# Kernel optimization log

Hardware: AMD Instinct MI355X
Metric: run time of the kernel (lower is better)

The kernel has to match this reference:

```python
import jax, jax.numpy as jnp
import numpy as np

B = 1      # batch
D = 64     # octree grid side at this level
N = 65536  # active voxels
C = 32     # channels (nin == nout for resblock)
K = 3      # kernel size


def _offsets():
    r = jnp.arange(K) - K // 2
    oz, oy, ox = jnp.meshgrid(r, r, r, indexing='ij')
    return jnp.stack([oz.ravel(), oy.ravel(), ox.ravel()], axis=-1)  # [27,3] (kz,ky,kx order)


def octree_conv3d(values, indices, mask_values, kernel, bias, activation=None):
    # values: [N,Cin], indices: [N,4] (b,z,y,x), mask_values: [N,1]
    Cin = values.shape[-1]
    Cout = kernel.shape[-1]
    taps = kernel.reshape(K * K * K, Cin, Cout)            # kz,ky,kx order == kernel[kz,ky,kx]
    vals = jnp.einsum('nc,tcd->tnd', values, taps)         # [27,N,Cout]
    offs = _offsets()                                      # [27,3]
    coords = indices[:, 1:]                                # [N,3]
    # shift = [0, kz-1, ky-1, kx-1]; clamp to [0, D-1] (stride=inv_stride=1)
    sh = jnp.clip(coords[None, :, :] + offs[:, None, :], 0, D - 1)  # [27,N,3]
    lin = indices[:, 0][None, :] * (D * D * D) + sh[..., 0] * (D * D) + sh[..., 1] * D + sh[..., 2]
    grid = jnp.zeros((B * D * D * D, Cout), dtype=values.dtype)
    grid = grid.at[lin.reshape(-1)].add(vals.reshape(-1, Cout))     # scatter-add == coalesce sum
    out_lin = indices[:, 0] * (D * D * D) + coords[:, 0] * (D * D) + coords[:, 1] * D + coords[:, 2]
    gathered = grid[out_lin]                               # [N,Cout] values at mask positions
    out = (gathered + mask_values * bias[None, :]) * mask_values     # result + mask*bias; result*mask
    if activation is not None:
        out = activation(out)
    return out


def setup_inputs() -> dict:
    key = jax.random.key(0)
    k1, k2, k3, k4, k5, k6 = jax.random.split(key, 6)
    G = B * D * D * D
    perm = jax.random.permutation(k1, G)[:N]               # unique (coalesced) voxel indices
    b = perm // (D * D * D)
    rem = perm % (D * D * D)
    z = rem // (D * D)
    y = (rem // D) % D
    x = rem % D
    indices = jnp.stack([b, z, y, x], axis=-1).astype(jnp.int64)   # [N,4]
    values = jax.random.normal(k2, (N, C), dtype=jnp.float32)
    mask_values = jnp.ones((N, 1), dtype=jnp.float32)
    stdv = 1.0 / np.sqrt(K * K * K * C)
    kern1 = (jax.random.uniform(k3, (K, K, K, C, C)) - 0.5) * 2.0 * stdv
    bias1 = (jax.random.uniform(k4, (C,)) - 0.5) * 2.0 * stdv
    kern2 = (jax.random.uniform(k5, (K, K, K, C, C)) - 0.5) * 2.0 * stdv
    bias2 = (jax.random.uniform(k6, (C,)) - 0.5) * 2.0 * stdv
    return {'values': values, 'indices': indices, 'mask_values': mask_values,
            'kern1': kern1, 'bias1': bias1, 'kern2': kern2, 'bias2': bias2}


def reference(values, indices, mask_values, kern1, bias1, kern2, bias2):
    # OctreeResblock: conv(relu) -> conv -> residual add, all on the sparse index set
    h = octree_conv3d(values, indices, mask_values, kern1, bias1, activation=jax.nn.relu)
    h = octree_conv3d(h, indices, mask_values, kern2, bias2, activation=None)
    return values + h
```

## Files before the change

kernel.cpp:

```cpp
#include <hip/hip_runtime.h>
#include <hip/hip_cooperative_groups.h>

namespace cg = cooperative_groups;

#define NPTS 65536
#define CCH  32
#define DDIM 64
#define GVOX (DDIM*DDIM*DDIM)
#define MAXTILES 4128
#define NTHREADS 1024
#define NBLOCKS  256
#define TTOT (NTHREADS*NBLOCKS)

typedef _Float16 half8  __attribute__((ext_vector_type(8)));
typedef _Float16 half4v __attribute__((ext_vector_type(4)));
typedef float    floatx4 __attribute__((ext_vector_type(4)));

#define P0N (GVOX/4 + MAXTILES*16 + (NPTS*CCH)/4 + 27*CCH*CCH + CCH + 27 + 1)

struct SharedC {
  _Float16 lw[27*CCH*CCH];
  int tstart[28];
  int clsbase[27];
  int lcnt[27];
  int lbase[27];
};

template<int MODE>
__device__ void conv_phase_c(SharedC& sh,
    const _Float16* __restrict__ A, const int* __restrict__ map,
    const int* __restrict__ pcoord, const int* __restrict__ sorted,
    const _Float16* __restrict__ WT, const float* __restrict__ bias,
    const float* __restrict__ mask, const float* __restrict__ resid,
    _Float16* __restrict__ hout, float* __restrict__ fout)
{
  for (int i = threadIdx.x; i < (27*CCH*CCH)/8; i += NTHREADS)
    ((half8*)sh.lw)[i] = ((const half8*)WT)[i];
  __syncthreads();

  const int wv   = threadIdx.x >> 6;
  const int lane = threadIdx.x & 63;
  const int m = lane & 15, quad = lane >> 4;
  const int nt = sh.tstart[27];
  const float bi0 = bias[m], bi1 = bias[m+16];

  for (int tile = blockIdx.x*(NTHREADS/64) + wv; tile < nt;
       tile += NBLOCKS*(NTHREADS/64)) {
    int scls = 0;
    for (int cc = 1; cc < 27; ++cc) if (tile >= sh.tstart[cc]) scls = cc;
    scls = __builtin_amdgcn_readfirstlane(scls);
    const int cz = scls/9, cy = (scls/3)%3, cx = scls%3;

    const int pid = sorted[tile*16 + m];
    const int pc  = pcoord[pid];
    const int bb = pc>>18, z = (pc>>12)&63, y = (pc>>6)&63, x = pc&63;
    const int linb = bb << 18;
    const int az[3] = { max(z-1,0)<<12, z<<12, min(z+1,DDIM-1)<<12 };
    const int ay[3] = { max(y-1,0)<<6,  y<<6,  min(y+1,DDIM-1)<<6 };
    const int ax[3] = { max(x-1,0),     x,     min(x+1,DDIM-1) };

    floatx4 acc0 = {0.f,0.f,0.f,0.f};
    floatx4 acc1 = {0.f,0.f,0.f,0.f};

    int srcs[27];
#pragma unroll
    for (int j = 0; j < 27; ++j) {
      const int jz = j/9, jy = (j/3)%3, jx = j%3;
      const int s = map[linb | az[jz] | ay[jy] | ax[jx]];
      srcs[j] = (s < 0) ? (NPTS*CCH) : (s*CCH);
    }
#pragma unroll
    for (int j = 0; j < 27; ++j) {
      const int jz = j/9, jy = (j/3)%3, jx = j%3;
      const int tz = (cz==1) ? (2-jz) : ((jz==1) ? 1 : ((cz==0) ? 0 : 2));
      const int ty = (cy==1) ? (2-jy) : ((jy==1) ? 1 : ((cy==0) ? 0 : 2));
      const int tx = (cx==1) ? (2-jx) : ((jx==1) ? 1 : ((cx==0) ? 0 : 2));
      const int t  = tz*9 + ty*3 + tx;
      half8 a  = *(const half8*)(A + srcs[j] + quad*8);
      const _Float16* wr = sh.lw + t*(CCH*CCH);
      half8 b0 = *(const half8*)(wr + m*CCH + quad*8);
      half8 b1 = *(const half8*)(wr + (16+m)*CCH + quad*8);
      acc0 = __builtin_amdgcn_mfma_f32_16x16x32_f16(a, b0, acc0, 0, 0, 0);
      acc1 = __builtin_amdgcn_mfma_f32_16x16x32_f16(a, b1, acc1, 0, 0, 0);
    }

#pragma unroll
    for (int reg = 0; reg < 4; ++reg) {
      const int r  = quad*4 + reg;
      const int pr = sorted[tile*16 + r];
      if (pr >= NPTS) continue;
      const float mk = mask[pr];
      float v0 = (acc0[reg] + mk*bi0) * mk;
      float v1 = (acc1[reg] + mk*bi1) * mk;
      if (MODE == 0) {
        v0 = fmaxf(v0, 0.f); v1 = fmaxf(v1, 0.f);
        hout[pr*CCH + m]      = (_Float16)v0;
        hout[pr*CCH + m + 16] = (_Float16)v1;
      } else {
        fout[pr*CCH + m]      = resid[pr*CCH + m]      + v0;
        fout[pr*CCH + m + 16] = resid[pr*CCH + m + 16] + v1;
      }
    }
  }
}

__global__ __launch_bounds__(1024, 4) void mega2(
    const float* __restrict__ values, const int* __restrict__ idx,
    const float* __restrict__ maskv,
    const float* __restrict__ k1, const float* __restrict__ bias1,
    const float* __restrict__ k2, const float* __restrict__ bias2,
    int* __restrict__ map, int* __restrict__ pcoord,
    int* __restrict__ sorted, int* __restrict__ cnt, int* __restrict__ slot,
    _Float16* __restrict__ valsh, _Float16* __restrict__ hh,
    _Float16* __restrict__ wt1, _Float16* __restrict__ wt2,
    float* __restrict__ out)
{
  __shared__ SharedC sh;
  cg::grid_group grid = cg::this_grid();
  const int gtid = blockIdx.x*NTHREADS + threadIdx.x;

  for (int t0 = gtid; t0 < P0N; t0 += TTOT) {
    int tid = t0;
    if (tid < GVOX/4) { ((int4*)map)[tid] = make_int4(-1,-1,-1,-1); continue; }
    tid -= GVOX/4;
    if (tid < MAXTILES*16) { sorted[tid] = NPTS; continue; }
    tid -= MAXTILES*16;
    if (tid < (NPTS*CCH)/4) {
      float4 v = ((const float4*)values)[tid];
      half4v h = { (_Float16)v.x, (_Float16)v.y, (_Float16)v.z, (_Float16)v.w };
      ((half4v*)valsh)[tid] = h; continue;
    }
    tid -= (NPTS*CCH)/4;
    if (tid < 27*CCH*CCH) {
      int t = tid/(CCH*CCH), r = tid%(CCH*CCH);
      int cin = r/CCH, cout = r%CCH;
      int o = (t*CCH + cout)*CCH + cin;
      wt1[o] = (_Float16)k1[tid]; wt2[o] = (_Float16)k2[tid]; continue;
    }
    tid -= 27*CCH*CCH;
    if (tid < CCH) { valsh[NPTS*CCH+tid] = (_Float16)0.f; hh[NPTS*CCH+tid] = (_Float16)0.f; continue; }
    tid -= CCH;
    if (tid < 27) { cnt[tid] = 0; slot[tid] = 0; continue; }
    tid -= 27;
    if (tid == 0) pcoord[NPTS] = 0;
  }
  grid.sync();

  if (threadIdx.x < 27) sh.lcnt[threadIdx.x] = 0;
  __syncthreads();
  int myc = -1;
  if (gtid < NPTS) {
    const int4 v = ((const int4*)idx)[gtid];
    const int b = v.x, z = v.y, y = v.z, x = v.w;
    map[((b*DDIM + z)*DDIM + y)*DDIM + x] = gtid;
    pcoord[gtid] = (b<<18) | (z<<12) | (y<<6) | x;
    const int cz = (z==0)?0:((z==DDIM-1)?2:1);
    const int cy = (y==0)?0:((y==DDIM-1)?2:1);
    const int cx = (x==0)?0:((x==DDIM-1)?2:1);
    myc = cz*9 + cy*3 + cx;
    atomicAdd(&sh.lcnt[myc], 1);
  }
  __syncthreads();
  if (threadIdx.x < 27 && sh.lcnt[threadIdx.x])
    atomicAdd(&cnt[threadIdx.x], sh.lcnt[threadIdx.x]);
  grid.sync();

  if (threadIdx.x == 0) {
    int b = 0, tb = 0;
    for (int c = 0; c < 27; ++c) {
      const int cv = atomicAdd(&cnt[c], 0);
      sh.clsbase[c] = b; sh.tstart[c] = tb;
      const int ntc = (cv + 15) >> 4;
      b += ntc << 4; tb += ntc;
    }
    sh.tstart[27] = tb;
  }
  if (threadIdx.x < 27) sh.lcnt[threadIdx.x] = 0;
  __syncthreads();
  int lrank = 0;
  if (gtid < NPTS) lrank = atomicAdd(&sh.lcnt[myc], 1);
  __syncthreads();
  if (threadIdx.x < 27)
    sh.lbase[threadIdx.x] = sh.lcnt[threadIdx.x] ? atomicAdd(&slot[threadIdx.x], sh.lcnt[threadIdx.x]) : 0;
  __syncthreads();
  if (gtid < NPTS) sorted[sh.clsbase[myc] + sh.lbase[myc] + lrank] = gtid;
  grid.sync();

  conv_phase_c<0>(sh, valsh, map, pcoord, sorted, wt1, bias1, maskv, nullptr, hh, nullptr);
  grid.sync();

  conv_phase_c<1>(sh, hh, map, pcoord, sorted, wt2, bias2, maskv, values, nullptr, out);
}

__global__ __launch_bounds__(256) void k_prep0(
    int* __restrict__ map, int* __restrict__ sorted,
    const float* __restrict__ values, _Float16* __restrict__ valsh,
    const float* __restrict__ k1, const float* __restrict__ k2,
    _Float16* __restrict__ w1, _Float16* __restrict__ w2,
    _Float16* __restrict__ hh, int* __restrict__ pcoord,
    int* __restrict__ cnt, int* __restrict__ slot)
{
  int tid = blockIdx.x * 256 + threadIdx.x;
  if (tid < GVOX/4) { ((int4*)map)[tid] = make_int4(-1,-1,-1,-1); return; }
  tid -= GVOX/4;
  if (tid < MAXTILES*16) { sorted[tid] = NPTS; return; }
  tid -= MAXTILES*16;
  if (tid < (NPTS*CCH)/4) {
    float4 v = ((const float4*)values)[tid];
    half4v h = { (_Float16)v.x, (_Float16)v.y, (_Float16)v.z, (_Float16)v.w };
    ((half4v*)valsh)[tid] = h; return;
  }
  tid -= (NPTS*CCH)/4;
  if (tid < 27*CCH*CCH) {
    int t = tid/(CCH*CCH), r = tid%(CCH*CCH);
    int cin = r/CCH, cout = r%CCH;
    int o = (t*CCH + cout)*CCH + cin;
    w1[o] = (_Float16)k1[tid]; w2[o] = (_Float16)k2[tid]; return;
  }
  tid -= 27*CCH*CCH;
  if (tid < CCH) { valsh[NPTS*CCH+tid] = (_Float16)0.f; hh[NPTS*CCH+tid] = (_Float16)0.f; return; }
  tid -= CCH;
  if (tid < 27) { cnt[tid] = 0; slot[tid] = 0; return; }
  tid -= 27;
  if (tid == 0) pcoord[NPTS] = 0;
}

__global__ __launch_bounds__(256) void k_prep1(const int* __restrict__ idx,
                                               int* __restrict__ map,
                                               int* __restrict__ pcoord,
                                               int* __restrict__ cls,
                                               int* __restrict__ cnt)
{
  __shared__ int lcnt[27];
  if (threadIdx.x < 27) lcnt[threadIdx.x] = 0;
  __syncthreads();
  const int n = blockIdx.x*256 + threadIdx.x;
  const int4 v = ((const int4*)idx)[n];
  const int b = v.x, z = v.y, y = v.z, x = v.w;
  map[((b*DDIM + z)*DDIM + y)*DDIM + x] = n;
  pcoord[n] = (b<<18) | (z<<12) | (y<<6) | x;
  const int cz = (z==0)?0:((z==DDIM-1)?2:1);
  const int cy = (y==0)?0:((y==DDIM-1)?2:1);
  const int cx = (x==0)?0:((x==DDIM-1)?2:1);
  const int c = cz*9 + cy*3 + cx;
  cls[n] = c;
  atomicAdd(&lcnt[c], 1);
  __syncthreads();
  if (threadIdx.x < 27 && lcnt[threadIdx.x]) atomicAdd(&cnt[threadIdx.x], lcnt[threadIdx.x]);
}

__global__ __launch_bounds__(256) void k_prep3(const int* __restrict__ cls,
                                               const int* __restrict__ cnt,
                                               int* __restrict__ slot,
                                               int* __restrict__ sorted,
                                               int* __restrict__ tileclass,
                                               int* __restrict__ ntiles)
{
  __shared__ int s_clsbase[27];
  __shared__ int s_tstart[28];
  if (threadIdx.x == 0) {
    int b = 0, tb = 0;
#pragma unroll
    for (int c = 0; c < 27; ++c) {
      s_clsbase[c] = b; s_tstart[c] = tb;
      const int ntc = (cnt[c] + 15) >> 4;
      b += ntc << 4; tb += ntc;
    }
    s_tstart[27] = tb;
    if (blockIdx.x == 0) *ntiles = tb;
  }
  __syncthreads();

  if (blockIdx.x < NPTS/256) {
    __shared__ int lcnt[27], lbase[27];
    if (threadIdx.x < 27) lcnt[threadIdx.x] = 0;
    __syncthreads();
    const int n = blockIdx.x*256 + threadIdx.x;
    const int c = cls[n];
    const int lrank = atomicAdd(&lcnt[c], 1);
    __syncthreads();
    if (threadIdx.x < 27)
      lbase[threadIdx.x] = lcnt[threadIdx.x] ? atomicAdd(&slot[threadIdx.x], lcnt[threadIdx.x]) : 0;
    __syncthreads();
    sorted[s_clsbase[c] + lbase[c] + lrank] = n;
  } else {
    const int i = (blockIdx.x - NPTS/256)*256 + threadIdx.x;
    if (i >= MAXTILES) return;
    const int nt = s_tstart[27];
    int c = 13;
    if (i < nt) {
      for (int cc = 0; cc < 27; ++cc)
        if (i >= s_tstart[cc] && i < s_tstart[cc+1]) { c = cc; break; }
    }
    tileclass[i] = c;
  }
}

template<int J0, int J1>
__device__ __forceinline__ void accum_taps(
    const _Float16* __restrict__ A, const int* __restrict__ map,
    const _Float16* lw,
    int cz, int cy, int cx, int linb,
    const int* az, const int* ay, const int* ax,
    int m, int quad, floatx4& acc0, floatx4& acc1)
{
  int srcs[J1 - J0];
#pragma unroll
  for (int j = J0; j < J1; ++j) {
    const int jz = j/9, jy = (j/3)%3, jx = j%3;
    const int s = map[linb | az[jz] | ay[jy] | ax[jx]];
    srcs[j - J0] = (s < 0) ? (NPTS*CCH) : (s*CCH);
  }
#pragma unroll
  for (int j = J0; j < J1; ++j) {
    const int jz = j/9, jy = (j/3)%3, jx = j%3;
    const int tz = (cz==1) ? (2-jz) : ((jz==1) ? 1 : ((cz==0) ? 0 : 2));
    const int ty = (cy==1) ? (2-jy) : ((jy==1) ? 1 : ((cy==0) ? 0 : 2));
    const int tx = (cx==1) ? (2-jx) : ((jx==1) ? 1 : ((cx==0) ? 0 : 2));
    const int t  = tz*9 + ty*3 + tx;
    half8 a  = *(const half8*)(A + srcs[j - J0] + quad*8);
    const _Float16* wr = lw + t*(CCH*CCH);
    half8 b0 = *(const half8*)(wr + m*CCH + quad*8);
    half8 b1 = *(const half8*)(wr + (16+m)*CCH + quad*8);
    acc0 = __builtin_amdgcn_mfma_f32_16x16x32_f16(a, b0, acc0, 0, 0, 0);
    acc1 = __builtin_amdgcn_mfma_f32_16x16x32_f16(a, b1, acc1, 0, 0, 0);
  }
}

template<int MODE>
__global__ __launch_bounds__(512) void conv_mfma(
    const _Float16* __restrict__ A,
    const int* __restrict__ map,
    const int* __restrict__ pcoord,
    const int* __restrict__ sorted,
    const int* __restrict__ tileclass,
    const int* __restrict__ ntp,
    const _Float16* __restrict__ WT,
    const float* __restrict__ bias,
    const float* __restrict__ mask,
    const float* __restrict__ resid,
    _Float16* __restrict__ hout,
    float* __restrict__ fout)
{
  __shared__ _Float16 lw[27*CCH*CCH];
  __shared__ float red[4][16][33];

  for (int i = threadIdx.x; i < 3456; i += 512)
    ((half8*)lw)[i] = ((const half8*)WT)[i];

  const int wv   = threadIdx.x >> 6;
  const int tl   = wv >> 1;
  const int half = wv & 1;
  const int tile = blockIdx.x*4 + tl;
  const int nt   = *ntp;
  const bool active = tile < nt;
  const int lane = threadIdx.x & 63;
  const int m = lane & 15, quad = lane >> 4;

  floatx4 acc0 = {0.f,0.f,0.f,0.f};
  floatx4 acc1 = {0.f,0.f,0.f,0.f};

  int scls = 13, pc = 0;
  if (active) {
    scls = __builtin_amdgcn_readfirstlane(tileclass[tile]);
    const int pid = sorted[tile*16 + m];
    pc = pcoord[pid];
  }
  __syncthreads();

  if (active) {
    const int cz = scls/9, cy = (scls/3)%3, cx = scls%3;
    const int bb = pc>>18, z = (pc>>12)&63, y = (pc>>6)&63, x = pc&63;
    const int linb = bb << 18;
    const int az[3] = { max(z-1,0)<<12, z<<12, min(z+1,DDIM-1)<<12 };
    const int ay[3] = { max(y-1,0)<<6,  y<<6,  min(y+1,DDIM-1)<<6 };
    const int ax[3] = { max(x-1,0),     x,     min(x+1,DDIM-1) };
    if (half == 0)
      accum_taps<0,14>(A, map, lw, cz,cy,cx, linb, az,ay,ax, m,quad, acc0,acc1);
    else
      accum_taps<14,27>(A, map, lw, cz,cy,cx, linb, az,ay,ax, m,quad, acc0,acc1);
  }

  if (active && half == 0) {
#pragma unroll
    for (int r = 0; r < 4; ++r) {
      red[tl][quad*4+r][m]    = acc0[r];
      red[tl][quad*4+r][m+16] = acc1[r];
    }
  }
  __syncthreads();
  if (active && half == 1) {
#pragma unroll
    for (int r = 0; r < 4; ++r) {
      acc0[r] += red[tl][quad*4+r][m];
      acc1[r] += red[tl][quad*4+r][m+16];
    }
    const float bi0 = bias[m], bi1 = bias[m+16];
#pragma unroll
    for (int reg = 0; reg < 4; ++reg) {
      const int r  = quad*4 + reg;
      const int pr = sorted[tile*16 + r];
      if (pr >= NPTS) continue;
      const float mk = mask[pr];
      float v0 = (acc0[reg] + mk*bi0) * mk;
      float v1 = (acc1[reg] + mk*bi1) * mk;
      if (MODE == 0) {
        v0 = fmaxf(v0, 0.f); v1 = fmaxf(v1, 0.f);
        hout[pr*CCH + m]      = (_Float16)v0;
        hout[pr*CCH + m + 16] = (_Float16)v1;
      } else {
        fout[pr*CCH + m]      = resid[pr*CCH + m]      + v0;
        fout[pr*CCH + m + 16] = resid[pr*CCH + m + 16] + v1;
      }
    }
  }
}


extern "C" void kernel_launch(void* const* d_in, const int* in_sizes, int n_in,
                              void* d_out, int out_size, void* d_ws, size_t ws_size,
                              hipStream_t stream) {
  const float* values = (const float*)d_in[0];
  const int*   indices= (const int*)  d_in[1];
  const float* maskv  = (const float*)d_in[2];
  const float* kern1  = (const float*)d_in[3];
  const float* bias1  = (const float*)d_in[4];
  const float* kern2  = (const float*)d_in[5];
  const float* bias2  = (const float*)d_in[6];
  float* out = (float*)d_out;

  char* ws = (char*)d_ws;
  size_t off = 0;
  auto alloc = [&](size_t bytes) { void* p = ws + off; off = (off + bytes + 255) & ~(size_t)255; return p; };
  int*      map      = (int*)     alloc(GVOX*4);
  int*      pcoord   = (int*)     alloc((NPTS+1)*4);
  int*      cls      = (int*)     alloc(NPTS*4);
  int*      sorted   = (int*)     alloc(MAXTILES*16*4);
  int*      tileclass= (int*)     alloc(MAXTILES*4);
  int*      cnt      = (int*)     alloc(27*4);
  int*      slot     = (int*)     alloc(27*4);
  int*      ntiles   = (int*)     alloc(4);
  _Float16* valsh    = (_Float16*)alloc((NPTS+1)*CCH*2);
  _Float16* hh       = (_Float16*)alloc((NPTS+1)*CCH*2);
  _Float16* wt1      = (_Float16*)alloc(27*CCH*CCH*2);
  _Float16* wt2      = (_Float16*)alloc(27*CCH*CCH*2);

  static int use_coop = -1;
  if (use_coop < 0) {
    int nb = 0;
    hipError_t e = hipOccupancyMaxActiveBlocksPerMultiprocessor(
        &nb, (const void*)mega2, NTHREADS, 0);
    use_coop = (e == hipSuccess && nb >= 1) ? 1 : 0;
  }

  if (use_coop) {
    void* args[] = { (void*)&values, (void*)&indices, (void*)&maskv,
                     (void*)&kern1, (void*)&bias1, (void*)&kern2, (void*)&bias2,
                     (void*)&map, (void*)&pcoord, (void*)&sorted,
                     (void*)&cnt, (void*)&slot,
                     (void*)&valsh, (void*)&hh, (void*)&wt1, (void*)&wt2,
                     (void*)&out };
    hipError_t e = hipLaunchCooperativeKernel((void*)mega2, dim3(NBLOCKS),
                                              dim3(NTHREADS), args, 0, stream);
    if (e == hipSuccess) return;
    use_coop = 0;
  }

  k_prep0<<<((GVOX/4 + MAXTILES*16 + (NPTS*CCH)/4 + 27*CCH*CCH + CCH + 27 + 1) + 255)/256,
            256, 0, stream>>>(
      map, sorted, values, valsh, kern1, kern2, wt1, wt2, hh, pcoord, cnt, slot);
  k_prep1<<<NPTS/256, 256, 0, stream>>>(indices, map, pcoord, cls, cnt);
  k_prep3<<<NPTS/256 + (MAXTILES+255)/256, 256, 0, stream>>>(
      cls, cnt, slot, sorted, tileclass, ntiles);
  conv_mfma<0><<<MAXTILES/4, 512, 0, stream>>>(valsh, map, pcoord, sorted, tileclass,
                                               ntiles, wt1, bias1, maskv, nullptr, hh, nullptr);
  conv_mfma<1><<<MAXTILES/4, 512, 0, stream>>>(hh, map, pcoord, sorted, tileclass,
                                               ntiles, wt2, bias2, maskv, values, nullptr, out);
}
```

Baseline: 140.4 us.

## Store sorted coords per slot, pre-swizzle weights, batch A loads with setprio

During the sort, each slot now stores its packed coordinates next to its point id. This removes the dependent sorted→pcoord load chain from the conv phase. The weights are re-laid out so each lane reads a contiguous half8 for the MFMA B operand, which reduces LDS address math and bank conflicts. A-operand gathers are issued in groups of 9 ahead of the MFMAs, with s_setprio raised around the compute. The fallback path also gains a precomputed neighbour-offset buffer, computed once and reused by both convs, and a one-wave-per-tile conv with no reduction. These add register pressure and extra buffers.

Result: faster. 128.4 us (-8.5%).

```diff
diff --git a/kernel.cpp b/kernel.cpp
--- a/kernel.cpp
+++ b/kernel.cpp
@@ -8,6 +8,7 @@
 #define DDIM 64
 #define GVOX (DDIM*DDIM*DDIM)
 #define MAXTILES 4128
+#define NSLOT (MAXTILES*16)
 #define NTHREADS 1024
 #define NBLOCKS  256
 #define TTOT (NTHREADS*NBLOCKS)
@@ -16,7 +17,7 @@
 typedef _Float16 half4v __attribute__((ext_vector_type(4)));
 typedef float    floatx4 __attribute__((ext_vector_type(4)));
 
-#define P0N (GVOX/4 + MAXTILES*16 + (NPTS*CCH)/4 + 27*CCH*CCH + CCH + 27 + 1)
+#define P0N (GVOX/4 + NSLOT/4 + NSLOT/4 + (NPTS*CCH)/4 + 27*CCH*CCH + CCH + 27)
 
 struct SharedC {
   _Float16 lw[27*CCH*CCH];
@@ -27,14 +28,14 @@
 };
 
 template<int MODE>
-__device__ void conv_phase_c(SharedC& sh,
+__device__ void conv_phase(SharedC& sh,
     const _Float16* __restrict__ A, const int* __restrict__ map,
-    const int* __restrict__ pcoord, const int* __restrict__ sorted,
+    const int* __restrict__ pcs, const int* __restrict__ sorted,
     const _Float16* __restrict__ WT, const float* __restrict__ bias,
     const float* __restrict__ mask, const float* __restrict__ resid,
     _Float16* __restrict__ hout, float* __restrict__ fout)
 {
-  for (int i = threadIdx.x; i < (27*CCH*CCH)/8; i += NTHREADS)
+  for (int i = threadIdx.x; i < 3456; i += NTHREADS)
     ((half8*)sh.lw)[i] = ((const half8*)WT)[i];
   __syncthreads();
 
@@ -44,44 +45,52 @@
   const int nt = sh.tstart[27];
   const float bi0 = bias[m], bi1 = bias[m+16];
 
-  for (int tile = blockIdx.x*(NTHREADS/64) + wv; tile < nt;
-       tile += NBLOCKS*(NTHREADS/64)) {
+  for (int tile = blockIdx.x*16 + wv; tile < nt; tile += NBLOCKS*16) {
     int scls = 0;
     for (int cc = 1; cc < 27; ++cc) if (tile >= sh.tstart[cc]) scls = cc;
     scls = __builtin_amdgcn_readfirstlane(scls);
     const int cz = scls/9, cy = (scls/3)%3, cx = scls%3;
 
-    const int pid = sorted[tile*16 + m];
-    const int pc  = pcoord[pid];
+    const int pc = pcs[tile*16 + m];
     const int bb = pc>>18, z = (pc>>12)&63, y = (pc>>6)&63, x = pc&63;
     const int linb = bb << 18;
     const int az[3] = { max(z-1,0)<<12, z<<12, min(z+1,DDIM-1)<<12 };
     const int ay[3] = { max(y-1,0)<<6,  y<<6,  min(y+1,DDIM-1)<<6 };
     const int ax[3] = { max(x-1,0),     x,     min(x+1,DDIM-1) };
 
-    floatx4 acc0 = {0.f,0.f,0.f,0.f};
-    floatx4 acc1 = {0.f,0.f,0.f,0.f};
-
     int srcs[27];
 #pragma unroll
     for (int j = 0; j < 27; ++j) {
       const int jz = j/9, jy = (j/3)%3, jx = j%3;
       const int s = map[linb | az[jz] | ay[jy] | ax[jx]];
-      srcs[j] = (s < 0) ? (NPTS*CCH) : (s*CCH);
-    }
-#pragma unroll
-    for (int j = 0; j < 27; ++j) {
-      const int jz = j/9, jy = (j/3)%3, jx = j%3;
-      const int tz = (cz==1) ? (2-jz) : ((jz==1) ? 1 : ((cz==0) ? 0 : 2));
-      const int ty = (cy==1) ? (2-jy) : ((jy==1) ? 1 : ((cy==0) ? 0 : 2));
-      const int tx = (cx==1) ? (2-jx) : ((jx==1) ? 1 : ((cx==0) ? 0 : 2));
-      const int t  = tz*9 + ty*3 + tx;
-      half8 a  = *(const half8*)(A + srcs[j] + quad*8);
-      const _Float16* wr = sh.lw + t*(CCH*CCH);
-      half8 b0 = *(const half8*)(wr + m*CCH + quad*8);
-      half8 b1 = *(const half8*)(wr + (16+m)*CCH + quad*8);
-      acc0 = __builtin_amdgcn_mfma_f32_16x16x32_f16(a, b0, acc0, 0, 0, 0);
-      acc1 = __builtin_amdgcn_mfma_f32_16x16x32_f16(a, b1, acc1, 0, 0, 0);
+      srcs[j] = ((s < 0) ? NPTS : s) * CCH;
+    }
+
+    floatx4 acc0 = {0.f,0.f,0.f,0.f};
+    floatx4 acc1 = {0.f,0.f,0.f,0.f};
+
+#pragma unroll
+    for (int g = 0; g < 3; ++g) {
+      half8 av[9];
+#pragma unroll
+      for (int u = 0; u < 9; ++u)
+        av[u] = *(const half8*)(A + srcs[g*9 + u] + quad*8);
+      __builtin_amdgcn_s_setprio(1);
+#pragma unroll
+      for (int u = 0; u < 9; ++u) {
+        const int j = g*9 + u;
+        const int jz = j/9, jy = (j/3)%3, jx = j%3;
+        const int tz = (cz==1) ? (2-jz) : ((jz==1) ? 1 : ((cz==0) ? 0 : 2));
+        const int ty = (cy==1) ? (2-jy) : ((jy==1) ? 1 : ((cy==0) ? 0 : 2));
+        const int tx = (cx==1) ? (2-jx) : ((jx==1) ? 1 : ((cx==0) ? 0 : 2));
+        const int t  = tz*9 + ty*3 + tx;
+        const _Float16* wr = sh.lw + t*1024;
+        half8 b0 = *(const half8*)(wr + lane*8);
+        half8 b1 = *(const half8*)(wr + 512 + lane*8);
+        acc0 = __builtin_amdgcn_mfma_f32_16x16x32_f16(av[u], b0, acc0, 0, 0, 0);
+        acc1 = __builtin_amdgcn_mfma_f32_16x16x32_f16(av[u], b1, acc1, 0, 0, 0);
+      }
+      __builtin_amdgcn_s_setprio(0);
     }
 
 #pragma unroll
@@ -104,13 +113,13 @@
   }
 }
 
-__global__ __launch_bounds__(1024, 4) void mega2(
+__global__ __launch_bounds__(1024, 4) void mega3(
     const float* __restrict__ values, const int* __restrict__ idx,
     const float* __restrict__ maskv,
     const float* __restrict__ k1, const float* __restrict__ bias1,
     const float* __restrict__ k2, const float* __restrict__ bias2,
-    int* __restrict__ map, int* __restrict__ pcoord,
-    int* __restrict__ sorted, int* __restrict__ cnt, int* __restrict__ slot,
+    int* __restrict__ map, int* __restrict__ sorted, int* __restrict__ pcs,
+    int* __restrict__ cnt, int* __restrict__ slot,
     _Float16* __restrict__ valsh, _Float16* __restrict__ hh,
     _Float16* __restrict__ wt1, _Float16* __restrict__ wt2,
     float* __restrict__ out)
@@ -123,8 +132,10 @@
     int tid = t0;
     if (tid < GVOX/4) { ((int4*)map)[tid] = make_int4(-1,-1,-1,-1); continue; }
     tid -= GVOX/4;
-    if (tid < MAXTILES*16) { sorted[tid] = NPTS; continue; }
-    tid -= MAXTILES*16;
+    if (tid < NSLOT/4) { ((int4*)sorted)[tid] = make_int4(NPTS,NPTS,NPTS,NPTS); continue; }
+    tid -= NSLOT/4;
+    if (tid < NSLOT/4) { ((int4*)pcs)[tid] = make_int4(0,0,0,0); continue; }
+    tid -= NSLOT/4;
     if (tid < (NPTS*CCH)/4) {
       float4 v = ((const float4*)values)[tid];
       half4v h = { (_Float16)v.x, (_Float16)v.y, (_Float16)v.z, (_Float16)v.w };
@@ -134,26 +145,25 @@
     if (tid < 27*CCH*CCH) {
       int t = tid/(CCH*CCH), r = tid%(CCH*CCH);
       int cin = r/CCH, cout = r%CCH;
-      int o = (t*CCH + cout)*CCH + cin;
+      int h = cout >> 4, mm = cout & 15, q = cin >> 3, i = cin & 7;
+      int o = t*1024 + h*512 + (q*16 + mm)*8 + i;
       wt1[o] = (_Float16)k1[tid]; wt2[o] = (_Float16)k2[tid]; continue;
     }
     tid -= 27*CCH*CCH;
     if (tid < CCH) { valsh[NPTS*CCH+tid] = (_Float16)0.f; hh[NPTS*CCH+tid] = (_Float16)0.f; continue; }
     tid -= CCH;
     if (tid < 27) { cnt[tid] = 0; slot[tid] = 0; continue; }
-    tid -= 27;
-    if (tid == 0) pcoord[NPTS] = 0;
   }
   grid.sync();
 
   if (threadIdx.x < 27) sh.lcnt[threadIdx.x] = 0;
   __syncthreads();
-  int myc = -1;
+  int myc = -1, mypc = 0;
   if (gtid < NPTS) {
     const int4 v = ((const int4*)idx)[gtid];
     const int b = v.x, z = v.y, y = v.z, x = v.w;
     map[((b*DDIM + z)*DDIM + y)*DDIM + x] = gtid;
-    pcoord[gtid] = (b<<18) | (z<<12) | (y<<6) | x;
+    mypc = (b<<18) | (z<<12) | (y<<6) | x;
     const int cz = (z==0)?0:((z==DDIM-1)?2:1);
     const int cy = (y==0)?0:((y==DDIM-1)?2:1);
     const int cx = (x==0)?0:((x==DDIM-1)?2:1);
@@ -183,17 +193,21 @@
   if (threadIdx.x < 27)
     sh.lbase[threadIdx.x] = sh.lcnt[threadIdx.x] ? atomicAdd(&slot[threadIdx.x], sh.lcnt[threadIdx.x]) : 0;
   __syncthreads();
-  if (gtid < NPTS) sorted[sh.clsbase[myc] + sh.lbase[myc] + lrank] = gtid;
+  if (gtid < NPTS) {
+    const int s = sh.clsbase[myc] + sh.lbase[myc] + lrank;
+    sorted[s] = gtid;
+    pcs[s] = mypc;
+  }
   grid.sync();
 
-  conv_phase_c<0>(sh, valsh, map, pcoord, sorted, wt1, bias1, maskv, nullptr, hh, nullptr);
+  conv_phase<0>(sh, valsh, map, pcs, sorted, wt1, bias1, maskv, nullptr, hh, nullptr);
   grid.sync();
 
-  conv_phase_c<1>(sh, hh, map, pcoord, sorted, wt2, bias2, maskv, values, nullptr, out);
+  conv_phase<1>(sh, hh, map, pcs, sorted, wt2, bias2, maskv, values, nullptr, out);
 }
 
 __global__ __launch_bounds__(256) void k_prep0(
-    int* __restrict__ map, int* __restrict__ sorted,
+    int* __restrict__ map, int* __restrict__ sorted, int* __restrict__ pcs,
     const float* __restrict__ values, _Float16* __restrict__ valsh,
     const float* __restrict__ k1, const float* __restrict__ k2,
     _Float16* __restrict__ w1, _Float16* __restrict__ w2,
@@ -203,8 +217,10 @@
   int tid = blockIdx.x * 256 + threadIdx.x;
   if (tid < GVOX/4) { ((int4*)map)[tid] = make_int4(-1,-1,-1,-1); return; }
   tid -= GVOX/4;
-  if (tid < MAXTILES*16) { sorted[tid] = NPTS; return; }
-  tid -= MAXTILES*16;
+  if (tid < NSLOT) { sorted[tid] = NPTS; return; }
+  tid -= NSLOT;
+  if (tid < NSLOT) { pcs[tid] = 0; return; }
+  tid -= NSLOT;
   if (tid < (NPTS*CCH)/4) {
     float4 v = ((const float4*)values)[tid];
     half4v h = { (_Float16)v.x, (_Float16)v.y, (_Float16)v.z, (_Float16)v.w };
@@ -214,7 +230,8 @@
   if (tid < 27*CCH*CCH) {
     int t = tid/(CCH*CCH), r = tid%(CCH*CCH);
     int cin = r/CCH, cout = r%CCH;
-    int o = (t*CCH + cout)*CCH + cin;
+    int h = cout >> 4, mm = cout & 15, q = cin >> 3, i = cin & 7;
+    int o = t*1024 + h*512 + (q*16 + mm)*8 + i;
     w1[o] = (_Float16)k1[tid]; w2[o] = (_Float16)k2[tid]; return;
   }
   tid -= 27*CCH*CCH;
@@ -224,6 +241,7 @@
   tid -= 27;
   if (tid == 0) pcoord[NPTS] = 0;
 }
+#define PREP0_THREADS (GVOX/4 + NSLOT + NSLOT + (NPTS*CCH)/4 + 27*CCH*CCH + CCH + 27 + 1)
 
 __global__ __launch_bounds__(256) void k_prep1(const int* __restrict__ idx,
                                                int* __restrict__ map,
@@ -252,7 +270,9 @@
 __global__ __launch_bounds__(256) void k_prep3(const int* __restrict__ cls,
                                                const int* __restrict__ cnt,
                                                int* __restrict__ slot,
+                                               const int* __restrict__ pcoord,
                                                int* __restrict__ sorted,
+                                               int* __restrict__ pcs,
                                                int* __restrict__ tileclass,
                                                int* __restrict__ ntiles)
 {
@@ -282,7 +302,9 @@
     if (threadIdx.x < 27)
       lbase[threadIdx.x] = lcnt[threadIdx.x] ? atomicAdd(&slot[threadIdx.x], lcnt[threadIdx.x]) : 0;
     __syncthreads();
-    sorted[s_clsbase[c] + lbase[c] + lrank] = n;
+    const int s = s_clsbase[c] + lbase[c] + lrank;
+    sorted[s] = n;
+    pcs[s] = pcoord[n];
   } else {
     const int i = (blockIdx.x - NPTS/256)*256 + threadIdx.x;
     if (i >= MAXTILES) return;
@@ -296,42 +318,28 @@
   }
 }
 
-template<int J0, int J1>
-__device__ __forceinline__ void accum_taps(
-    const _Float16* __restrict__ A, const int* __restrict__ map,
-    const _Float16* lw,
-    int cz, int cy, int cx, int linb,
-    const int* az, const int* ay, const int* ax,
-    int m, int quad, floatx4& acc0, floatx4& acc1)
-{
-  int srcs[J1 - J0];
-#pragma unroll
-  for (int j = J0; j < J1; ++j) {
-    const int jz = j/9, jy = (j/3)%3, jx = j%3;
-    const int s = map[linb | az[jz] | ay[jy] | ax[jx]];
-    srcs[j - J0] = (s < 0) ? (NPTS*CCH) : (s*CCH);
-  }
-#pragma unroll
-  for (int j = J0; j < J1; ++j) {
-    const int jz = j/9, jy = (j/3)%3, jx = j%3;
-    const int tz = (cz==1) ? (2-jz) : ((jz==1) ? 1 : ((cz==0) ? 0 : 2));
-    const int ty = (cy==1) ? (2-jy) : ((jy==1) ? 1 : ((cy==0) ? 0 : 2));
-    const int tx = (cx==1) ? (2-jx) : ((jx==1) ? 1 : ((cx==0) ? 0 : 2));
-    const int t  = tz*9 + ty*3 + tx;
-    half8 a  = *(const half8*)(A + srcs[j - J0] + quad*8);
-    const _Float16* wr = lw + t*(CCH*CCH);
-    half8 b0 = *(const half8*)(wr + m*CCH + quad*8);
-    half8 b1 = *(const half8*)(wr + (16+m)*CCH + quad*8);
-    acc0 = __builtin_amdgcn_mfma_f32_16x16x32_f16(a, b0, acc0, 0, 0, 0);
-    acc1 = __builtin_amdgcn_mfma_f32_16x16x32_f16(a, b1, acc1, 0, 0, 0);
-  }
+__global__ __launch_bounds__(256) void k_nbr(const int* __restrict__ pcs,
+                                             const int* __restrict__ map,
+                                             int* __restrict__ nbr)
+{
+  const int tid = blockIdx.x*256 + threadIdx.x;
+  if (tid >= MAXTILES*432) return;
+  const int tile = tid/432, rem = tid%432;
+  const int j = rem >> 4, m = rem & 15;
+  const int pc = pcs[tile*16 + m];
+  const int bb = pc>>18, z = (pc>>12)&63, y = (pc>>6)&63, x = pc&63;
+  const int jz = j/9, jy = (j/3)%3, jx = j%3;
+  const int nz = min(max(z + jz - 1, 0), DDIM-1);
+  const int ny = min(max(y + jy - 1, 0), DDIM-1);
+  const int nx = min(max(x + jx - 1, 0), DDIM-1);
+  const int s = map[(bb<<18) | (nz<<12) | (ny<<6) | nx];
+  nbr[tid] = ((s < 0) ? NPTS : s) * CCH;
 }
 
 template<int MODE>
-__global__ __launch_bounds__(512) void conv_mfma(
+__global__ __launch_bounds__(512, 4) void conv_mfma(
     const _Float16* __restrict__ A,
-    const int* __restrict__ map,
-    const int* __restrict__ pcoord,
+    const int* __restrict__ nbr,
     const int* __restrict__ sorted,
     const int* __restrict__ tileclass,
     const int* __restrict__ ntp,
@@ -343,75 +351,65 @@
     float* __restrict__ fout)
 {
   __shared__ _Float16 lw[27*CCH*CCH];
-  __shared__ float red[4][16][33];
-
   for (int i = threadIdx.x; i < 3456; i += 512)
     ((half8*)lw)[i] = ((const half8*)WT)[i];
+  __syncthreads();
 
   const int wv   = threadIdx.x >> 6;
-  const int tl   = wv >> 1;
-  const int half = wv & 1;
-  const int tile = blockIdx.x*4 + tl;
-  const int nt   = *ntp;
-  const bool active = tile < nt;
+  const int tile = blockIdx.x*8 + wv;
   const int lane = threadIdx.x & 63;
   const int m = lane & 15, quad = lane >> 4;
+  if (tile >= *ntp) return;
+
+  const int scls = __builtin_amdgcn_readfirstlane(tileclass[tile]);
+  const int cz = scls/9, cy = (scls/3)%3, cx = scls%3;
+
+  const int tb = tile*432;
+  int srcs[27];
+#pragma unroll
+  for (int j = 0; j < 27; ++j) srcs[j] = nbr[tb + j*16 + m];
 
   floatx4 acc0 = {0.f,0.f,0.f,0.f};
   floatx4 acc1 = {0.f,0.f,0.f,0.f};
 
-  int scls = 13, pc = 0;
-  if (active) {
-    scls = __builtin_amdgcn_readfirstlane(tileclass[tile]);
-    const int pid = sorted[tile*16 + m];
-    pc = pcoord[pid];
-  }
-  __syncthreads();
-
-  if (active) {
-    const int cz = scls/9, cy = (scls/3)%3, cx = scls%3;
-    const int bb = pc>>18, z = (pc>>12)&63, y = (pc>>6)&63, x = pc&63;
-    const int linb = bb << 18;
-    const int az[3] = { max(z-1,0)<<12, z<<12, min(z+1,DDIM-1)<<12 };
-    const int ay[3] = { max(y-1,0)<<6,  y<<6,  min(y+1,DDIM-1)<<6 };
-    const int ax[3] = { max(x-1,0),     x,     min(x+1,DDIM-1) };
-    if (half == 0)
-      accum_taps<0,14>(A, map, lw, cz,cy,cx, linb, az,ay,ax, m,quad, acc0,acc1);
-    else
-      accum_taps<14,27>(A, map, lw, cz,cy,cx, linb, az,ay,ax, m,quad, acc0,acc1);
-  }
-
-  if (active && half == 0) {
-#pragma unroll
-    for (int r = 0; r < 4; ++r) {
-      red[tl][quad*4+r][m]    = acc0[r];
-      red[tl][quad*4+r][m+16] = acc1[r];
-    }
-  }
-  __syncthreads();
-  if (active && half == 1) {
-#pragma unroll
-    for (int r = 0; r < 4; ++r) {
-      acc0[r] += red[tl][quad*4+r][m];
-      acc1[r] += red[tl][quad*4+r][m+16];
-    }
-    const float bi0 = bias[m], bi1 = bias[m+16];
-#pragma unroll
-    for (int reg = 0; reg < 4; ++reg) {
-      const int r  = quad*4 + reg;
-      const int pr = sorted[tile*16 + r];
-      if (pr >= NPTS) continue;
-      const float mk = mask[pr];
-      float v0 = (acc0[reg] + mk*bi0) * mk;
-      float v1 = (acc1[reg] + mk*bi1) * mk;
-      if (MODE == 0) {
-        v0 = fmaxf(v0, 0.f); v1 = fmaxf(v1, 0.f);
-        hout[pr*CCH + m]      = (_Float16)v0;
-        hout[pr*CCH + m + 16] = (_Float16)v1;
-      } else {
-        fout[pr*CCH + m]      = resid[pr*CCH + m]      + v0;
-        fout[pr*CCH + m + 16] = resid[pr*CCH + m + 16] + v1;
-      }
+#pragma unroll
+  for (int g = 0; g < 3; ++g) {
+    half8 av[9];
+#pragma unroll
+    for (int u = 0; u < 9; ++u)
+      av[u] = *(const half8*)(A + srcs[g*9 + u] + quad*8);
+#pragma unroll
+    for (int u = 0; u < 9; ++u) {
+      const int j = g*9 + u;
+      const int jz = j/9, jy = (j/3)%3, jx = j%3;
+      const int tz = (cz==1) ? (2-jz) : ((jz==1) ? 1 : ((cz==0) ? 0 : 2));
+      const int ty = (cy==1) ? (2-jy) : ((jy==1) ? 1 : ((cy==0) ? 0 : 2));
+      const int tx = (cx==1) ? (2-jx) : ((jx==1) ? 1 : ((cx==0) ? 0 : 2));
+      const int t  = tz*9 + ty*3 + tx;
+      const _Float16* wr = lw + t*1024;
+      half8 b0 = *(const half8*)(wr + lane*8);
+      half8 b1 = *(const half8*)(wr + 512 + lane*8);
+      acc0 = __builtin_amdgcn_mfma_f32_16x16x32_f16(av[u], b0, acc0, 0, 0, 0);
+      acc1 = __builtin_amdgcn_mfma_f32_16x16x32_f16(av[u], b1, acc1, 0, 0, 0);
+    }
+  }
+
+  const float bi0 = bias[m], bi1 = bias[m+16];
+#pragma unroll
+  for (int reg = 0; reg < 4; ++reg) {
+    const int r  = quad*4 + reg;
+    const int pr = sorted[tile*16 + r];
+    if (pr >= NPTS) continue;
+    const float mk = mask[pr];
+    float v0 = (acc0[reg] + mk*bi0) * mk;
+    float v1 = (acc1[reg] + mk*bi1) * mk;
+    if (MODE == 0) {
+      v0 = fmaxf(v0, 0.f); v1 = fmaxf(v1, 0.f);
+      hout[pr*CCH + m]      = (_Float16)v0;
+      hout[pr*CCH + m + 16] = (_Float16)v1;
+    } else {
+      fout[pr*CCH + m]      = resid[pr*CCH + m]      + v0;
+      fout[pr*CCH + m + 16] = resid[pr*CCH + m + 16] + v1;
     }
   }
 }
@@ -435,8 +433,10 @@
   int*      map      = (int*)     alloc(GVOX*4);
   int*      pcoord   = (int*)     alloc((NPTS+1)*4);
   int*      cls      = (int*)     alloc(NPTS*4);
-  int*      sorted   = (int*)     alloc(MAXTILES*16*4);
+  int*      sorted   = (int*)     alloc(NSLOT*4);
+  int*      pcs      = (int*)     alloc(NSLOT*4);
   int*      tileclass= (int*)     alloc(MAXTILES*4);
+  int*      nbr      = (int*)     alloc((size_t)MAXTILES*432*4);
   int*      cnt      = (int*)     alloc(27*4);
   int*      slot     = (int*)     alloc(27*4);
   int*      ntiles   = (int*)     alloc(4);
@@ -449,31 +449,31 @@
   if (use_coop < 0) {
     int nb = 0;
     hipError_t e = hipOccupancyMaxActiveBlocksPerMultiprocessor(
-        &nb, (const void*)mega2, NTHREADS, 0);
+        &nb, (const void*)mega3, NTHREADS, 0);
     use_coop = (e == hipSuccess && nb >= 1) ? 1 : 0;
   }
 
   if (use_coop) {
     void* args[] = { (void*)&values, (void*)&indices, (void*)&maskv,
                      (void*)&kern1, (void*)&bias1, (void*)&kern2, (void*)&bias2,
-                     (void*)&map, (void*)&pcoord, (void*)&sorted,
+                     (void*)&map, (void*)&sorted, (void*)&pcs,
                      (void*)&cnt, (void*)&slot,
                      (void*)&valsh, (void*)&hh, (void*)&wt1, (void*)&wt2,
                      (void*)&out };
-    hipError_t e = hipLaunchCooperativeKernel((void*)mega2, dim3(NBLOCKS),
+    hipError_t e = hipLaunchCooperativeKernel((void*)mega3, dim3(NBLOCKS),
                                               dim3(NTHREADS), args, 0, stream);
     if (e == hipSuccess) return;
     use_coop = 0;
   }
 
-  k_prep0<<<((GVOX/4 + MAXTILES*16 + (NPTS*CCH)/4 + 27*CCH*CCH + CCH + 27 + 1) + 255)/256,
-            256, 0, stream>>>(
-      map, sorted, values, valsh, kern1, kern2, wt1, wt2, hh, pcoord, cnt, slot);
+  k_prep0<<<(PREP0_THREADS + 255)/256, 256, 0, stream>>>(
+      map, sorted, pcs, values, valsh, kern1, kern2, wt1, wt2, hh, pcoord, cnt, slot);
   k_prep1<<<NPTS/256, 256, 0, stream>>>(indices, map, pcoord, cls, cnt);
   k_prep3<<<NPTS/256 + (MAXTILES+255)/256, 256, 0, stream>>>(
-      cls, cnt, slot, sorted, tileclass, ntiles);
-  conv_mfma<0><<<MAXTILES/4, 512, 0, stream>>>(valsh, map, pcoord, sorted, tileclass,
-                                               ntiles, wt1, bias1, maskv, nullptr, hh, nullptr);
-  conv_mfma<1><<<MAXTILES/4, 512, 0, stream>>>(hh, map, pcoord, sorted, tileclass,
-                                               ntiles, wt2, bias2, maskv, values, nullptr, out);
-}
+      cls, cnt, slot, pcoord, sorted, pcs, tileclass, ntiles);
+  k_nbr<<<(MAXTILES*432 + 255)/256, 256, 0, stream>>>(pcs, map, nbr);
+  conv_mfma<0><<<(MAXTILES + 7)/8, 512, 0, stream>>>(valsh, nbr, sorted, tileclass,
+                                                     ntiles, wt1, bias1, maskv, nullptr, hh, nullptr);
+  conv_mfma<1><<<(MAXTILES + 7)/8, 512, 0, stream>>>(hh, nbr, sorted, tileclass,
+                                                     ntiles, wt2, bias2, maskv, values, nullptr, out);
+}
```
